# Optimization experiments

Measured on AMD Instinct MI355X. Metric: run time of the kernel, lower is better.

The kernel has to match this reference:

```python
import jax, jax.numpy as jnp
import numpy as np

B, C, T = 64, 512, 1000
BR = 3
RED = 1
H = C // RED


def setup_inputs() -> dict:
    key = jax.random.key(0)
    ks = jax.random.split(key, 8)
    x0 = jax.random.normal(ks[0], (B, C, T), dtype=jnp.float32)
    x1 = jax.random.normal(ks[1], (B, C, T), dtype=jnp.float32)
    x2 = jax.random.normal(ks[2], (B, C, T), dtype=jnp.float32)
    # linear1: Conv1d(2C -> H, kernel 1) == dense [H, 2C]
    W1 = jax.random.normal(ks[3], (H, 2 * C), dtype=jnp.float32) * (1.0 / np.sqrt(2 * C))
    b1 = jnp.zeros((H,), dtype=jnp.float32)
    # linear2: BR branch convs Conv1d(H -> C, kernel 1), stacked: [BR, C, H]
    W2 = jax.random.normal(ks[4], (BR, C, H), dtype=jnp.float32) * (1.0 / np.sqrt(H))
    b2 = jnp.zeros((BR, C), dtype=jnp.float32)
    return {"x0": x0, "x1": x1, "x2": x2, "W1": W1, "b1": b1, "W2": W2, "b2": b2}


def reference(x0, x1, x2, W1, b1, W2, b2):
    # f: [B, BR, C, T]
    f = jnp.stack([x0, x1, x2], axis=1)
    xs = f.sum(axis=1)  # [B, C, T]
    t = xs.shape[-1]
    mean = xs.mean(axis=-1)  # [B, C]
    # unbiased std (torch.std default)
    var = ((xs - mean[..., None]) ** 2).sum(axis=-1) / (t - 1)
    std = jnp.sqrt(var)
    stats = jnp.concatenate([mean, std], axis=-1)  # [B, 2C]
    h = stats @ W1.T + b1  # [B, H]
    s = jnp.einsum('bh,kch->bkc', h, W2) + b2  # [B, BR, C]
    w = jax.nn.softmax(s, axis=1)[..., None]  # [B, BR, C, 1]
    return (f * w).sum(axis=1)  # [B, C, T]
```

## Files before the change

### kernel.cpp

```cpp
#include <hip/hip_runtime.h>
#include <math.h>

#define NB 64
#define NC 512
#define NT 1000
#define NH 512
#define TWOC 1024
#define NT4 250
#define TAIL 58

typedef float vfloat4 __attribute__((ext_vector_type(4)));

__global__ __launch_bounds__(256) void stats_kernel(const float* __restrict__ x0,
                                                    const float* __restrict__ x1,
                                                    const float* __restrict__ x2,
                                                    float* __restrict__ stats) {
    const int row  = blockIdx.x * 4 + (threadIdx.x >> 6);
    const int lane = threadIdx.x & 63;

    const float4* p0 = (const float4*)x0 + (size_t)row * NT4;
    const float4* p1 = (const float4*)x1 + (size_t)row * NT4;
    const float4* p2 = (const float4*)x2 + (size_t)row * NT4;

    const bool tail = lane < TAIL;
    const int  i3   = tail ? (192 + lane) : lane;
    const float m3  = tail ? 1.f : 0.f;

    const float4 a0 = p0[lane];
    const float4 a1 = p0[lane + 64];
    const float4 a2 = p0[lane + 128];
    const float4 a3 = p0[i3];
    const float4 b0 = p1[lane];
    const float4 b1 = p1[lane + 64];
    const float4 b2 = p1[lane + 128];
    const float4 b3 = p1[i3];
    const float4 c0 = p2[lane];
    const float4 c1 = p2[lane + 64];
    const float4 c2 = p2[lane + 128];
    const float4 c3 = p2[i3];
    __builtin_amdgcn_sched_barrier(0);

    float s0 = 0.f, q0 = 0.f, s1 = 0.f, q1 = 0.f;
    float s2 = 0.f, q2 = 0.f, s3 = 0.f, q3 = 0.f;
    float v;
    v = a0.x + b0.x + c0.x; s0 += v; q0 += v * v;
    v = a0.y + b0.y + c0.y; s0 += v; q0 += v * v;
    v = a0.z + b0.z + c0.z; s0 += v; q0 += v * v;
    v = a0.w + b0.w + c0.w; s0 += v; q0 += v * v;
    v = a1.x + b1.x + c1.x; s1 += v; q1 += v * v;
    v = a1.y + b1.y + c1.y; s1 += v; q1 += v * v;
    v = a1.z + b1.z + c1.z; s1 += v; q1 += v * v;
    v = a1.w + b1.w + c1.w; s1 += v; q1 += v * v;
    v = a2.x + b2.x + c2.x; s2 += v; q2 += v * v;
    v = a2.y + b2.y + c2.y; s2 += v; q2 += v * v;
    v = a2.z + b2.z + c2.z; s2 += v; q2 += v * v;
    v = a2.w + b2.w + c2.w; s2 += v; q2 += v * v;
    v = (a3.x + b3.x + c3.x) * m3; s3 += v; q3 += v * v;
    v = (a3.y + b3.y + c3.y) * m3; s3 += v; q3 += v * v;
    v = (a3.z + b3.z + c3.z) * m3; s3 += v; q3 += v * v;
    v = (a3.w + b3.w + c3.w) * m3; s3 += v; q3 += v * v;

    float s = (s0 + s1) + (s2 + s3);
    float sq = (q0 + q1) + (q2 + q3);

    #pragma unroll
    for (int off = 32; off; off >>= 1) {
        s  += __shfl_down(s,  off);
        sq += __shfl_down(sq, off);
    }
    if (lane == 0) {
        const float mean = s / (float)NT;
        const float var  = (sq - s * s / (float)NT) / (float)(NT - 1);
        const float sd   = sqrtf(fmaxf(var, 0.f));
        const int b = row >> 9;
        const int c = row & (NC - 1);
        stats[b * TWOC + c]      = mean;
        stats[b * TWOC + NC + c] = sd;
    }
}

__global__ __launch_bounds__(256) void h_kernel(const float* __restrict__ stats,
                                                const float* __restrict__ W1,
                                                const float* __restrict__ b1,
                                                float* __restrict__ hbuf) {
    const int wid  = blockIdx.x * 4 + (threadIdx.x >> 6);
    const int lane = threadIdx.x & 63;
    const int j    = wid >> 4;
    const int b0   = (wid & 15) * 4;

    const float4* wr  = (const float4*)(W1 + (size_t)j * TWOC);
    const float4* s0p = (const float4*)(stats + (size_t)(b0 + 0) * TWOC);
    const float4* s1p = (const float4*)(stats + (size_t)(b0 + 1) * TWOC);
    const float4* s2p = (const float4*)(stats + (size_t)(b0 + 2) * TWOC);
    const float4* s3p = (const float4*)(stats + (size_t)(b0 + 3) * TWOC);

    float a0 = 0.f, a1 = 0.f, a2 = 0.f, a3 = 0.f;
    #pragma unroll
    for (int r = 0; r < 4; ++r) {
        const int i4 = r * 64 + lane;
        const float4 wv = wr[i4];
        const float4 v0 = s0p[i4];
        const float4 v1 = s1p[i4];
        const float4 v2 = s2p[i4];
        const float4 v3 = s3p[i4];
        a0 += wv.x*v0.x + wv.y*v0.y + wv.z*v0.z + wv.w*v0.w;
        a1 += wv.x*v1.x + wv.y*v1.y + wv.z*v1.z + wv.w*v1.w;
        a2 += wv.x*v2.x + wv.y*v2.y + wv.z*v2.z + wv.w*v2.w;
        a3 += wv.x*v3.x + wv.y*v3.y + wv.z*v3.z + wv.w*v3.w;
    }
    #pragma unroll
    for (int off = 32; off; off >>= 1) {
        a0 += __shfl_down(a0, off);
        a1 += __shfl_down(a1, off);
        a2 += __shfl_down(a2, off);
        a3 += __shfl_down(a3, off);
    }
    if (lane == 0) {
        const float bb = b1[j];
        hbuf[(size_t)(b0 + 0) * NH + j] = a0 + bb;
        hbuf[(size_t)(b0 + 1) * NH + j] = a1 + bb;
        hbuf[(size_t)(b0 + 2) * NH + j] = a2 + bb;
        hbuf[(size_t)(b0 + 3) * NH + j] = a3 + bb;
    }
}

__global__ __launch_bounds__(256) void sw_kernel(const float* __restrict__ hbuf,
                                                 const float* __restrict__ W2,
                                                 const float* __restrict__ b2,
                                                 float* __restrict__ wbuf) {
    const int wid  = blockIdx.x * 4 + (threadIdx.x >> 6);
    const int lane = threadIdx.x & 63;
    const int c    = wid >> 4;
    const int b0   = (wid & 15) * 4;

    const float4* w0r = (const float4*)(W2 + ((size_t)(0 * NC + c)) * NH);
    const float4* w1r = (const float4*)(W2 + ((size_t)(1 * NC + c)) * NH);
    const float4* w2r = (const float4*)(W2 + ((size_t)(2 * NC + c)) * NH);

    float acc00=0,acc01=0,acc02=0,acc03=0;
    float acc10=0,acc11=0,acc12=0,acc13=0;
    float acc20=0,acc21=0,acc22=0,acc23=0;

    #pragma unroll
    for (int r = 0; r < 2; ++r) {
        const int i4 = r * 64 + lane;
        const float4 w0v = w0r[i4];
        const float4 w1v = w1r[i4];
        const float4 w2v = w2r[i4];
        const float4 h0 = ((const float4*)(hbuf + (size_t)(b0 + 0) * NH))[i4];
        const float4 h1 = ((const float4*)(hbuf + (size_t)(b0 + 1) * NH))[i4];
        const float4 h2 = ((const float4*)(hbuf + (size_t)(b0 + 2) * NH))[i4];
        const float4 h3 = ((const float4*)(hbuf + (size_t)(b0 + 3) * NH))[i4];
        acc00 += w0v.x*h0.x + w0v.y*h0.y + w0v.z*h0.z + w0v.w*h0.w;
        acc01 += w0v.x*h1.x + w0v.y*h1.y + w0v.z*h1.z + w0v.w*h1.w;
        acc02 += w0v.x*h2.x + w0v.y*h2.y + w0v.z*h2.z + w0v.w*h2.w;
        acc03 += w0v.x*h3.x + w0v.y*h3.y + w0v.z*h3.z + w0v.w*h3.w;
        acc10 += w1v.x*h0.x + w1v.y*h0.y + w1v.z*h0.z + w1v.w*h0.w;
        acc11 += w1v.x*h1.x + w1v.y*h1.y + w1v.z*h1.z + w1v.w*h1.w;
        acc12 += w1v.x*h2.x + w1v.y*h2.y + w1v.z*h2.z + w1v.w*h2.w;
        acc13 += w1v.x*h3.x + w1v.y*h3.y + w1v.z*h3.z + w1v.w*h3.w;
        acc20 += w2v.x*h0.x + w2v.y*h0.y + w2v.z*h0.z + w2v.w*h0.w;
        acc21 += w2v.x*h1.x + w2v.y*h1.y + w2v.z*h1.z + w2v.w*h1.w;
        acc22 += w2v.x*h2.x + w2v.y*h2.y + w2v.z*h2.z + w2v.w*h2.w;
        acc23 += w2v.x*h3.x + w2v.y*h3.y + w2v.z*h3.z + w2v.w*h3.w;
    }
    #pragma unroll
    for (int off = 32; off; off >>= 1) {
        acc00 += __shfl_down(acc00, off); acc01 += __shfl_down(acc01, off);
        acc02 += __shfl_down(acc02, off); acc03 += __shfl_down(acc03, off);
        acc10 += __shfl_down(acc10, off); acc11 += __shfl_down(acc11, off);
        acc12 += __shfl_down(acc12, off); acc13 += __shfl_down(acc13, off);
        acc20 += __shfl_down(acc20, off); acc21 += __shfl_down(acc21, off);
        acc22 += __shfl_down(acc22, off); acc23 += __shfl_down(acc23, off);
    }
    if (lane == 0) {
        const float bb0 = b2[0 * NC + c];
        const float bb1 = b2[1 * NC + c];
        const float bb2 = b2[2 * NC + c];
        float v0[4] = {acc00 + bb0, acc01 + bb0, acc02 + bb0, acc03 + bb0};
        float v1[4] = {acc10 + bb1, acc11 + bb1, acc12 + bb1, acc13 + bb1};
        float v2[4] = {acc20 + bb2, acc21 + bb2, acc22 + bb2, acc23 + bb2};
        #pragma unroll
        for (int bb = 0; bb < 4; ++bb) {
            const float m  = fmaxf(v0[bb], fmaxf(v1[bb], v2[bb]));
            const float e0 = expf(v0[bb] - m);
            const float e1 = expf(v1[bb] - m);
            const float e2 = expf(v2[bb] - m);
            const float inv = 1.f / (e0 + e1 + e2);
            const size_t base = (size_t)(b0 + bb) * 3 * NC + c;
            wbuf[base + 0 * NC] = e0 * inv;
            wbuf[base + 1 * NC] = e1 * inv;
            wbuf[base + 2 * NC] = e2 * inv;
        }
    }
}

__global__ __launch_bounds__(256) void apply_kernel(const float* __restrict__ x0,
                                                    const float* __restrict__ x1,
                                                    const float* __restrict__ x2,
                                                    const float* __restrict__ wbuf,
                                                    float* __restrict__ out) {
    const int rblk = (int)gridDim.x - 1 - (int)blockIdx.x;
    const int row  = rblk * 4 + (threadIdx.x >> 6);
    const int lane = threadIdx.x & 63;
    const int b = row >> 9;
    const int c = row & (NC - 1);

    const float4* p0 = (const float4*)x0 + (size_t)row * NT4;
    const float4* p1 = (const float4*)x1 + (size_t)row * NT4;
    const float4* p2 = (const float4*)x2 + (size_t)row * NT4;
    vfloat4*      po = (vfloat4*)out     + (size_t)row * NT4;

    const bool tail = lane < TAIL;
    const int  i3   = tail ? (192 + lane) : lane;

    const float w0 = wbuf[((size_t)b * 3 + 0) * NC + c];
    const float w1 = wbuf[((size_t)b * 3 + 1) * NC + c];
    const float w2 = wbuf[((size_t)b * 3 + 2) * NC + c];
    const float4 a0 = p0[lane];
    const float4 a1 = p0[lane + 64];
    const float4 a2 = p0[lane + 128];
    const float4 a3 = p0[i3];
    const float4 d0 = p1[lane];
    const float4 d1 = p1[lane + 64];
    const float4 d2 = p1[lane + 128];
    const float4 d3 = p1[i3];
    const float4 e0 = p2[lane];
    const float4 e1 = p2[lane + 64];
    const float4 e2 = p2[lane + 128];
    const float4 e3 = p2[i3];
    __builtin_amdgcn_sched_barrier(0);

    vfloat4 o;
    o.x = a0.x*w0 + d0.x*w1 + e0.x*w2;
    o.y = a0.y*w0 + d0.y*w1 + e0.y*w2;
    o.z = a0.z*w0 + d0.z*w1 + e0.z*w2;
    o.w = a0.w*w0 + d0.w*w1 + e0.w*w2;
    __builtin_nontemporal_store(o, &po[lane]);
    o.x = a1.x*w0 + d1.x*w1 + e1.x*w2;
    o.y = a1.y*w0 + d1.y*w1 + e1.y*w2;
    o.z = a1.z*w0 + d1.z*w1 + e1.z*w2;
    o.w = a1.w*w0 + d1.w*w1 + e1.w*w2;
    __builtin_nontemporal_store(o, &po[lane + 64]);
    o.x = a2.x*w0 + d2.x*w1 + e2.x*w2;
    o.y = a2.y*w0 + d2.y*w1 + e2.y*w2;
    o.z = a2.z*w0 + d2.z*w1 + e2.z*w2;
    o.w = a2.w*w0 + d2.w*w1 + e2.w*w2;
    __builtin_nontemporal_store(o, &po[lane + 128]);
    if (tail) {
        o.x = a3.x*w0 + d3.x*w1 + e3.x*w2;
        o.y = a3.y*w0 + d3.y*w1 + e3.y*w2;
        o.z = a3.z*w0 + d3.z*w1 + e3.z*w2;
        o.w = a3.w*w0 + d3.w*w1 + e3.w*w2;
        __builtin_nontemporal_store(o, &po[i3]);
    }
}

extern "C" void kernel_launch(void* const* d_in, const int* in_sizes, int n_in,
                              void* d_out, int out_size, void* d_ws, size_t ws_size,
                              hipStream_t stream) {
    const float* x0 = (const float*)d_in[0];
    const float* x1 = (const float*)d_in[1];
    const float* x2 = (const float*)d_in[2];
    const float* W1 = (const float*)d_in[3];
    const float* b1 = (const float*)d_in[4];
    const float* W2 = (const float*)d_in[5];
    const float* b2 = (const float*)d_in[6];
    float* out = (float*)d_out;

    float* stats = (float*)d_ws;
    float* hbuf  = stats + NB * TWOC;
    float* wbuf  = hbuf + NB * NH;

    stats_kernel<<<NB * NC / 4, 256, 0, stream>>>(x0, x1, x2, stats);
    h_kernel<<<2048, 256, 0, stream>>>(stats, W1, b1, hbuf);
    sw_kernel<<<2048, 256, 0, stream>>>(hbuf, W2, b2, wbuf);
    apply_kernel<<<NB * NC / 4, 256, 0, stream>>>(x0, x1, x2, wbuf, out);
}
```

Baseline: 169.8 us.

## Process four rows per wave in stats kernel with double-buffered loads

The stats kernel launches a quarter as many blocks and has each wave handle four rows strided by NWAVES. Row loads are double-buffered so the next row's global loads are issued before the current row is reduced, overlapping memory latency with compute and cutting block launch overhead. It doubles live registers per thread (two 12-float4 buffers), which may lower occupancy.

```diff
diff --git a/kernel.cpp b/kernel.cpp
--- a/kernel.cpp
+++ b/kernel.cpp
@@ -8,61 +8,50 @@
 #define TWOC 1024
 #define NT4 250
 #define TAIL 58
+#define NWAVES 8192
 
 typedef float vfloat4 __attribute__((ext_vector_type(4)));
 
-__global__ __launch_bounds__(256) void stats_kernel(const float* __restrict__ x0,
-                                                    const float* __restrict__ x1,
-                                                    const float* __restrict__ x2,
-                                                    float* __restrict__ stats) {
-    const int row  = blockIdx.x * 4 + (threadIdx.x >> 6);
-    const int lane = threadIdx.x & 63;
-
-    const float4* p0 = (const float4*)x0 + (size_t)row * NT4;
-    const float4* p1 = (const float4*)x1 + (size_t)row * NT4;
-    const float4* p2 = (const float4*)x2 + (size_t)row * NT4;
-
-    const bool tail = lane < TAIL;
-    const int  i3   = tail ? (192 + lane) : lane;
-    const float m3  = tail ? 1.f : 0.f;
-
-    const float4 a0 = p0[lane];
-    const float4 a1 = p0[lane + 64];
-    const float4 a2 = p0[lane + 128];
-    const float4 a3 = p0[i3];
-    const float4 b0 = p1[lane];
-    const float4 b1 = p1[lane + 64];
-    const float4 b2 = p1[lane + 128];
-    const float4 b3 = p1[i3];
-    const float4 c0 = p2[lane];
-    const float4 c1 = p2[lane + 64];
-    const float4 c2 = p2[lane + 128];
-    const float4 c3 = p2[i3];
-    __builtin_amdgcn_sched_barrier(0);
-
+struct RowBuf {
+    float4 a0, a1, a2, a3, b0, b1, b2, b3, c0, c1, c2, c3;
+};
+
+__device__ __forceinline__ void load_row(const float4* __restrict__ x0,
+                                         const float4* __restrict__ x1,
+                                         const float4* __restrict__ x2,
+                                         int row, int lane, int i3, RowBuf& r) {
+    const float4* p0 = x0 + (size_t)row * NT4;
+    const float4* p1 = x1 + (size_t)row * NT4;
+    const float4* p2 = x2 + (size_t)row * NT4;
+    r.a0 = p0[lane]; r.a1 = p0[lane + 64]; r.a2 = p0[lane + 128]; r.a3 = p0[i3];
+    r.b0 = p1[lane]; r.b1 = p1[lane + 64]; r.b2 = p1[lane + 128]; r.b3 = p1[i3];
+    r.c0 = p2[lane]; r.c1 = p2[lane + 64]; r.c2 = p2[lane + 128]; r.c3 = p2[i3];
+}
+
+__device__ __forceinline__ void reduce_row(const RowBuf& r, float m3, int lane, int row,
+                                           float* __restrict__ stats) {
     float s0 = 0.f, q0 = 0.f, s1 = 0.f, q1 = 0.f;
     float s2 = 0.f, q2 = 0.f, s3 = 0.f, q3 = 0.f;
     float v;
-    v = a0.x + b0.x + c0.x; s0 += v; q0 += v * v;
-    v = a0.y + b0.y + c0.y; s0 += v; q0 += v * v;
-    v = a0.z + b0.z + c0.z; s0 += v; q0 += v * v;
-    v = a0.w + b0.w + c0.w; s0 += v; q0 += v * v;
-    v = a1.x + b1.x + c1.x; s1 += v; q1 += v * v;
-    v = a1.y + b1.y + c1.y; s1 += v; q1 += v * v;
-    v = a1.z + b1.z + c1.z; s1 += v; q1 += v * v;
-    v = a1.w + b1.w + c1.w; s1 += v; q1 += v * v;
-    v = a2.x + b2.x + c2.x; s2 += v; q2 += v * v;
-    v = a2.y + b2.y + c2.y; s2 += v; q2 += v * v;
-    v = a2.z + b2.z + c2.z; s2 += v; q2 += v * v;
-    v = a2.w + b2.w + c2.w; s2 += v; q2 += v * v;
-    v = (a3.x + b3.x + c3.x) * m3; s3 += v; q3 += v * v;
-    v = (a3.y + b3.y + c3.y) * m3; s3 += v; q3 += v * v;
-    v = (a3.z + b3.z + c3.z) * m3; s3 += v; q3 += v * v;
-    v = (a3.w + b3.w + c3.w) * m3; s3 += v; q3 += v * v;
-
-    float s = (s0 + s1) + (s2 + s3);
+    v = r.a0.x + r.b0.x + r.c0.x; s0 += v; q0 += v * v;
+    v = r.a0.y + r.b0.y + r.c0.y; s0 += v; q0 += v * v;
+    v = r.a0.z + r.b0.z + r.c0.z; s0 += v; q0 += v * v;
+    v = r.a0.w + r.b0.w + r.c0.w; s0 += v; q0 += v * v;
+    v = r.a1.x + r.b1.x + r.c1.x; s1 += v; q1 += v * v;
+    v = r.a1.y + r.b1.y + r.c1.y; s1 += v; q1 += v * v;
+    v = r.a1.z + r.b1.z + r.c1.z; s1 += v; q1 += v * v;
+    v = r.a1.w + r.b1.w + r.c1.w; s1 += v; q1 += v * v;
+    v = r.a2.x + r.b2.x + r.c2.x; s2 += v; q2 += v * v;
+    v = r.a2.y + r.b2.y + r.c2.y; s2 += v; q2 += v * v;
+    v = r.a2.z + r.b2.z + r.c2.z; s2 += v; q2 += v * v;
+    v = r.a2.w + r.b2.w + r.c2.w; s2 += v; q2 += v * v;
+    v = (r.a3.x + r.b3.x + r.c3.x) * m3; s3 += v; q3 += v * v;
+    v = (r.a3.y + r.b3.y + r.c3.y) * m3; s3 += v; q3 += v * v;
+    v = (r.a3.z + r.b3.z + r.c3.z) * m3; s3 += v; q3 += v * v;
+    v = (r.a3.w + r.b3.w + r.c3.w) * m3; s3 += v; q3 += v * v;
+
+    float s  = (s0 + s1) + (s2 + s3);
     float sq = (q0 + q1) + (q2 + q3);
-
     #pragma unroll
     for (int off = 32; off; off >>= 1) {
         s  += __shfl_down(s,  off);
@@ -77,6 +66,35 @@
         stats[b * TWOC + c]      = mean;
         stats[b * TWOC + NC + c] = sd;
     }
+}
+
+__global__ __launch_bounds__(256) void stats_kernel(const float* __restrict__ x0f,
+                                                    const float* __restrict__ x1f,
+                                                    const float* __restrict__ x2f,
+                                                    float* __restrict__ stats) {
+    const int wid  = blockIdx.x * 4 + (threadIdx.x >> 6);
+    const int lane = threadIdx.x & 63;
+    const bool tail = lane < TAIL;
+    const int  i3   = tail ? (192 + lane) : lane;
+    const float m3  = tail ? 1.f : 0.f;
+
+    const float4* x0 = (const float4*)x0f;
+    const float4* x1 = (const float4*)x1f;
+    const float4* x2 = (const float4*)x2f;
+
+    RowBuf X, Y;
+    load_row(x0, x1, x2, wid, lane, i3, X);
+    __builtin_amdgcn_sched_barrier(0);
+    load_row(x0, x1, x2, wid + NWAVES, lane, i3, Y);
+    __builtin_amdgcn_sched_barrier(0);
+    reduce_row(X, m3, lane, wid, stats);
+    load_row(x0, x1, x2, wid + 2 * NWAVES, lane, i3, X);
+    __builtin_amdgcn_sched_barrier(0);
+    reduce_row(Y, m3, lane, wid + NWAVES, stats);
+    load_row(x0, x1, x2, wid + 3 * NWAVES, lane, i3, Y);
+    __builtin_amdgcn_sched_barrier(0);
+    reduce_row(X, m3, lane, wid + 2 * NWAVES, stats);
+    reduce_row(Y, m3, lane, wid + 3 * NWAVES, stats);
 }
 
 __global__ __launch_bounds__(256) void h_kernel(const float* __restrict__ stats,
@@ -272,7 +290,7 @@
     float* hbuf  = stats + NB * TWOC;
     float* wbuf  = hbuf + NB * NH;
 
-    stats_kernel<<<NB * NC / 4, 256, 0, stream>>>(x0, x1, x2, stats);
+    stats_kernel<<<NWAVES / 4, 256, 0, stream>>>(x0, x1, x2, stats);
     h_kernel<<<2048, 256, 0, stream>>>(stats, W1, b1, hbuf);
     sw_kernel<<<2048, 256, 0, stream>>>(hbuf, W2, b2, wbuf);
     apply_kernel<<<NB * NC / 4, 256, 0, stream>>>(x0, x1, x2, wbuf, out);
```

Result: slower. 173.6 us (+2.2%).
